# Performance work log

Measured on AMD Instinct MI355X. Metric: run time of the kernel, lower is better.

Reference implementation:

```python
import jax, jax.numpy as jnp
import numpy as np
import math

B, QL, HID = 4, 4, 4096          # batch, speculative q_len, hidden_size
NH, NKV, HD = 32, 8, 128         # attention heads, kv heads, head_dim
GROUPS = NH // NKV               # GQA repeat factor = 4
PRIOR = 4096                     # cached (prior) KV length
THETA = 1.0e6                    # Mixtral rope_theta


def setup_inputs() -> dict:
    key = jax.random.key(0)
    ks = jax.random.split(key, 7)
    hidden_states = jax.random.normal(ks[0], (B, QL, HID), jnp.float32)
    past_k = jax.random.normal(ks[1], (B, NKV, PRIOR, HD), jnp.float32)
    past_v = jax.random.normal(ks[2], (B, NKV, PRIOR, HD), jnp.float32)
    wq = jax.random.normal(ks[3], (HID, NH * HD), jnp.float32) * 0.02
    wk = jax.random.normal(ks[4], (HID, NKV * HD), jnp.float32) * 0.02
    wv = jax.random.normal(ks[5], (HID, NKV * HD), jnp.float32) * 0.02
    wo = jax.random.normal(ks[6], (NH * HD, HID), jnp.float32) * 0.02
    # prior mask: all cached positions visible
    attention_mask = jnp.ones((B, 1, QL, PRIOR), dtype=bool)
    # active mask: causal over the speculative window
    active_mask = jnp.broadcast_to(jnp.tril(jnp.ones((QL, QL), dtype=bool)), (B, 1, QL, QL))
    position_ids = jnp.broadcast_to(PRIOR + jnp.arange(QL, dtype=jnp.int64), (B, QL))
    return {"hidden_states": hidden_states, "past_k": past_k, "past_v": past_v,
            "wq": wq, "wk": wk, "wv": wv, "wo": wo,
            "attention_mask": attention_mask, "active_mask": active_mask,
            "position_ids": position_ids}


def _rotate_half(x):
    x1, x2 = jnp.split(x, 2, axis=-1)
    return jnp.concatenate([-x2, x1], axis=-1)


def _rope_cos_sin(position_ids):
    inv_freq = 1.0 / (THETA ** (jnp.arange(0, HD, 2, dtype=jnp.float32) / HD))  # [HD/2]
    freqs = position_ids.astype(jnp.float32)[..., None] * inv_freq              # [B,QL,HD/2]
    emb = jnp.concatenate([freqs, freqs], axis=-1)                              # [B,QL,HD]
    return jnp.cos(emb)[:, None], jnp.sin(emb)[:, None]                          # [B,1,QL,HD]


def reference(hidden_states, past_k, past_v, wq, wk, wv, wo,
              attention_mask, active_mask, position_ids):
    # fused QKV projection (no bias in Mixtral)
    q = (hidden_states @ wq).reshape(B, QL, NH, HD).transpose(0, 2, 1, 3)   # [B,NH,QL,HD]
    k = (hidden_states @ wk).reshape(B, QL, NKV, HD).transpose(0, 2, 1, 3)  # [B,NKV,QL,HD]
    v = (hidden_states @ wv).reshape(B, QL, NKV, HD).transpose(0, 2, 1, 3)
    # RoPE on Q and active K
    cos, sin = _rope_cos_sin(position_ids)
    q = q * cos + _rotate_half(q) * sin
    k = k * cos + _rotate_half(k) * sin
    # GQA repeat_kv
    k_prior = jnp.repeat(past_k, GROUPS, axis=1)  # [B,NH,PRIOR,HD]
    v_prior = jnp.repeat(past_v, GROUPS, axis=1)
    k_active = jnp.repeat(k, GROUPS, axis=1)      # [B,NH,QL,HD]
    v_active = jnp.repeat(v, GROUPS, axis=1)
    scale = 1.0 / math.sqrt(HD)
    neg = jnp.finfo(jnp.float32).min
    prior_scores = jnp.einsum('bhqd,bhkd->bhqk', q, k_prior) * scale
    prior_scores = jnp.where(attention_mask, prior_scores, neg)
    active_scores = jnp.einsum('bhqd,bhkd->bhqk', q, k_active) * scale
    active_scores = jnp.where(active_mask, active_scores, neg)   # is_speculation=True
    # decomposed softmax: shared max and shared divisor across prior/active
    max_score = jnp.maximum(prior_scores.max(-1, keepdims=True),
                            active_scores.max(-1, keepdims=True))
    prior_exp = jnp.exp(prior_scores - max_score)
    active_exp = jnp.exp(active_scores - max_score)
    divisor = prior_exp.sum(-1, keepdims=True) + active_exp.sum(-1, keepdims=True)
    attn = (jnp.einsum('bhqk,bhkd->bhqd', prior_exp / divisor, v_prior) +
            jnp.einsum('bhqk,bhkd->bhqd', active_exp / divisor, v_active))
    attn = attn.transpose(0, 2, 1, 3).reshape(B, QL, NH * HD)
    return attn @ wo
```

## Files before the change

kernel.cpp:

```cpp
#include <hip/hip_runtime.h>
#include <math.h>

#define NROWS 16
#define NCOLS 6144
#define HID   4096
#define NKV   8
#define HD    128
#define PRIOR 4096
#define NCH   32
#define CHUNK 128
#define SUB   64
#define KC1   128
#define NKC   32

__global__ __launch_bounds__(128)
void k_qkv_partial(const float* __restrict__ hid,
                   const float* __restrict__ wq,
                   const float* __restrict__ wk,
                   const float* __restrict__ wv,
                   float* __restrict__ part)
{
    const int t   = threadIdx.x;
    const int col = blockIdx.x * 256 + t * 2;
    const int kc  = blockIdx.y;
    const int k0  = kc * KC1;
    const float* w; int wn, wcol;
    if (col < 4096)      { w = wq; wn = 4096; wcol = col; }
    else if (col < 5120) { w = wk; wn = 1024; wcol = col - 4096; }
    else                 { w = wv; wn = 1024; wcol = col - 5120; }
    const float* wp = w + wcol + (size_t)k0 * wn;

    float acc[NROWS][2];
#pragma unroll
    for (int m = 0; m < NROWS; m++) { acc[m][0] = 0.f; acc[m][1] = 0.f; }
#pragma unroll 2
    for (int kk = 0; kk < KC1; kk += 4) {
        const float2 w0 = *(const float2*)(wp + (size_t)(kk + 0) * wn);
        const float2 w1 = *(const float2*)(wp + (size_t)(kk + 1) * wn);
        const float2 w2 = *(const float2*)(wp + (size_t)(kk + 2) * wn);
        const float2 w3 = *(const float2*)(wp + (size_t)(kk + 3) * wn);
#pragma unroll
        for (int m = 0; m < NROWS; m++) {
            const float4 h4 = *(const float4*)(hid + (size_t)m * HID + k0 + kk);
            acc[m][0] = fmaf(h4.x, w0.x, fmaf(h4.y, w1.x, fmaf(h4.z, w2.x, fmaf(h4.w, w3.x, acc[m][0]))));
            acc[m][1] = fmaf(h4.x, w0.y, fmaf(h4.y, w1.y, fmaf(h4.z, w2.y, fmaf(h4.w, w3.y, acc[m][1]))));
        }
    }
    float* po = part + (size_t)kc * (NROWS * NCOLS) + col;
#pragma unroll
    for (int m = 0; m < NROWS; m++)
        *(float2*)(po + (size_t)m * NCOLS) = make_float2(acc[m][0], acc[m][1]);
}

__global__ __launch_bounds__(256)
void k_reduce_rope(const float* __restrict__ part, float* __restrict__ qkv)
{
    const int tid = blockIdx.x * 256 + threadIdx.x;
    const double L64 = 0.21586735246819178;

    if (tid < 32768) {
        const int d = tid & 63, h = (tid >> 6) & 31, r = tid >> 11;
        const int c1 = h * HD + d;
        float s1 = 0.f, s2 = 0.f;
        for (int c = 0; c < NKC; c++) {
            const float* p = part + (size_t)c * (NROWS * NCOLS) + r * NCOLS + c1;
            s1 += p[0]; s2 += p[64];
        }
        const double ang = (double)(PRIOR + (r & 3)) * exp(-(double)d * L64);
        double sv, cv; sincos(ang, &sv, &cv);
        const float cf = (float)cv, sf = (float)sv, sc = 0.08838834764831845f;
        qkv[r * NCOLS + c1]      = (s1 * cf - s2 * sf) * sc;
        qkv[r * NCOLS + c1 + 64] = (s2 * cf + s1 * sf) * sc;
    } else if (tid < 40960) {
        const int idx = tid - 32768;
        const int d = idx & 63, kh = (idx >> 6) & 7, r = idx >> 9;
        const int c1 = 4096 + kh * HD + d;
        float s1 = 0.f, s2 = 0.f;
        for (int c = 0; c < NKC; c++) {
            const float* p = part + (size_t)c * (NROWS * NCOLS) + r * NCOLS + c1;
            s1 += p[0]; s2 += p[64];
        }
        const double ang = (double)(PRIOR + (r & 3)) * exp(-(double)d * L64);
        double sv, cv; sincos(ang, &sv, &cv);
        const float cf = (float)cv, sf = (float)sv;
        qkv[r * NCOLS + c1]      = s1 * cf - s2 * sf;
        qkv[r * NCOLS + c1 + 64] = s2 * cf + s1 * sf;
    } else {
        const int idx = tid - 40960;
        const int n = idx & 1023, r = idx >> 10;
        const int c1 = 5120 + n;
        float s = 0.f;
        for (int c = 0; c < NKC; c++)
            s += part[(size_t)c * (NROWS * NCOLS) + r * NCOLS + c1];
        qkv[r * NCOLS + c1] = s;
    }
}

__global__ __launch_bounds__(256, 4)
void k_attn_prior(const float* __restrict__ qkv,
                  const float* __restrict__ pk,
                  const float* __restrict__ pv,
                  float* __restrict__ part3)
{
    const int chunk = blockIdx.x, kvh = blockIdx.y, b = blockIdx.z;
    const int t = threadIdx.x;
    const int lane = t & 63;

    __shared__ float kT[128][64];
    __shared__ float qT[128][16];
    float* pP = &kT[88][0];
    float* aS = &kT[108][0];

    const int qt = t >> 6;
    const int h  = (lane >> 4) & 3;
    const int kt = lane & 15;

    const int d4pv = t & 31;
    const int kp   = (t >> 5) & 3;
    const int rh   = t >> 7;

    const size_t kvoff = ((size_t)(b * NKV + kvh) * PRIOR + (size_t)chunk * CHUNK) * HD;
    const float* kbase = pk + kvoff;
    const float* vbase = pv + kvoff;

    for (int i = t; i < 2048; i += 256) {
        const int r = i & 15, d = i >> 4;
        const int ql = r & 3, g = r >> 2;
        qT[d][r] = qkv[(size_t)(b * 4 + ql) * NCOLS + (kvh * 4 + g) * HD + d];
    }

    float m_r[4], l_r[4];
#pragma unroll
    for (int i = 0; i < 4; i++) { m_r[i] = -INFINITY; l_r[i] = 0.f; }
    float o[8][4];
#pragma unroll
    for (int jr = 0; jr < 8; jr++)
#pragma unroll
        for (int jd = 0; jd < 4; jd++) o[jr][jd] = 0.f;

    for (int st = 0; st < CHUNK / SUB; st++) {
        {
            const float* kr = kbase + (size_t)(st * SUB + lane) * HD + qt * 32;
#pragma unroll
            for (int i = 0; i < 8; i++) {
                const float4 k4 = *(const float4*)(kr + i * 4);
                const int d = qt * 32 + i * 4;
                kT[d + 0][lane] = k4.x; kT[d + 1][lane] = k4.y;
                kT[d + 2][lane] = k4.z; kT[d + 3][lane] = k4.w;
            }
        }
        __syncthreads();

        float a[4][4];
#pragma unroll
        for (int i = 0; i < 4; i++)
#pragma unroll
            for (int j = 0; j < 4; j++) a[i][j] = 0.f;
#pragma unroll 4
        for (int dd = 0; dd < 32; dd++) {
            const int d = h * 32 + dd;
            const float4 q4 = *(const float4*)(&qT[d][qt * 4]);
            const float4 k4 = *(const float4*)(&kT[d][kt * 4]);
            a[0][0]=fmaf(q4.x,k4.x,a[0][0]); a[0][1]=fmaf(q4.x,k4.y,a[0][1]); a[0][2]=fmaf(q4.x,k4.z,a[0][2]); a[0][3]=fmaf(q4.x,k4.w,a[0][3]);
            a[1][0]=fmaf(q4.y,k4.x,a[1][0]); a[1][1]=fmaf(q4.y,k4.y,a[1][1]); a[1][2]=fmaf(q4.y,k4.z,a[1][2]); a[1][3]=fmaf(q4.y,k4.w,a[1][3]);
            a[2][0]=fmaf(q4.z,k4.x,a[2][0]); a[2][1]=fmaf(q4.z,k4.y,a[2][1]); a[2][2]=fmaf(q4.z,k4.z,a[2][2]); a[2][3]=fmaf(q4.z,k4.w,a[2][3]);
            a[3][0]=fmaf(q4.w,k4.x,a[3][0]); a[3][1]=fmaf(q4.w,k4.y,a[3][1]); a[3][2]=fmaf(q4.w,k4.z,a[3][2]); a[3][3]=fmaf(q4.w,k4.w,a[3][3]);
        }
        __syncthreads();

#pragma unroll
        for (int i = 0; i < 4; i++)
#pragma unroll
            for (int j = 0; j < 4; j++) {
                float v = a[i][j];
                v += __shfl_xor(v, 16);
                v += __shfl_xor(v, 32);
                a[i][j] = v;
            }
        float al[4], pr[4][4];
#pragma unroll
        for (int i = 0; i < 4; i++) {
            float mx = fmaxf(fmaxf(a[i][0], a[i][1]), fmaxf(a[i][2], a[i][3]));
            mx = fmaxf(mx, __shfl_xor(mx, 1));
            mx = fmaxf(mx, __shfl_xor(mx, 2));
            mx = fmaxf(mx, __shfl_xor(mx, 4));
            mx = fmaxf(mx, __shfl_xor(mx, 8));
            const float mn = fmaxf(m_r[i], mx);
            al[i] = __expf(m_r[i] - mn);
            m_r[i] = mn;
            float s = 0.f;
#pragma unroll
            for (int j = 0; j < 4; j++) { pr[i][j] = __expf(a[i][j] - mn); s += pr[i][j]; }
            s += __shfl_xor(s, 1); s += __shfl_xor(s, 2);
            s += __shfl_xor(s, 4); s += __shfl_xor(s, 8);
            l_r[i] = l_r[i] * al[i] + s;
        }
        if (h == 0) {
#pragma unroll
            for (int j = 0; j < 4; j++)
                *(float4*)(pP + (kt * 4 + j) * 20 + qt * 4) =
                    make_float4(pr[0][j], pr[1][j], pr[2][j], pr[3][j]);
        }
        if (lane == 0) {
#pragma unroll
            for (int i = 0; i < 4; i++) aS[qt * 4 + i] = al[i];
        }
        __syncthreads();

        {
            float alv[8];
#pragma unroll
            for (int jr = 0; jr < 8; jr++) alv[jr] = aS[rh * 8 + jr];
#pragma unroll
            for (int jr = 0; jr < 8; jr++)
#pragma unroll
                for (int jd = 0; jd < 4; jd++) o[jr][jd] *= alv[jr];
            const float* vs = vbase + (size_t)st * SUB * HD + d4pv * 4;
#pragma unroll 4
            for (int j = 0; j < 16; j++) {
                const int key = kp * 16 + j;
                const float4 v4 = *(const float4*)(vs + (size_t)key * HD);
                const float4 pa = *(const float4*)(pP + key * 20 + rh * 8);
                const float4 pb = *(const float4*)(pP + key * 20 + rh * 8 + 4);
                const float pv8[8] = {pa.x, pa.y, pa.z, pa.w, pb.x, pb.y, pb.z, pb.w};
                const float vv[4] = {v4.x, v4.y, v4.z, v4.w};
#pragma unroll
                for (int jr = 0; jr < 8; jr++)
#pragma unroll
                    for (int jd = 0; jd < 4; jd++)
                        o[jr][jd] = fmaf(pv8[jr], vv[jd], o[jr][jd]);
            }
        }
        __syncthreads();
    }

    float* red = &kT[0][0];
    const int rb = (rh * 32 + d4pv) * 36;
    if (kp >= 2) {
        float* wdst = red + (kp - 2) * 2304 + rb;
#pragma unroll
        for (int jr = 0; jr < 8; jr++)
            *(float4*)(wdst + jr * 4) = make_float4(o[jr][0], o[jr][1], o[jr][2], o[jr][3]);
    }
    __syncthreads();
    if (kp < 2) {
        const float* rsrc = red + kp * 2304 + rb;
#pragma unroll
        for (int jr = 0; jr < 8; jr++) {
            const float4 x = *(const float4*)(rsrc + jr * 4);
            o[jr][0] += x.x; o[jr][1] += x.y; o[jr][2] += x.z; o[jr][3] += x.w;
        }
    }
    __syncthreads();
    if (kp == 1) {
        float* wdst = red + rb;
#pragma unroll
        for (int jr = 0; jr < 8; jr++)
            *(float4*)(wdst + jr * 4) = make_float4(o[jr][0], o[jr][1], o[jr][2], o[jr][3]);
    }
    __syncthreads();

    float* pout = part3 + (size_t)((b * NKV + kvh) * NCH + chunk) * 2080;
    if (lane == 0) {
#pragma unroll
        for (int i = 0; i < 4; i++) { pout[qt * 4 + i] = m_r[i]; pout[16 + qt * 4 + i] = l_r[i]; }
    }
    if (kp == 0) {
        const float* rsrc = red + rb;
#pragma unroll
        for (int jr = 0; jr < 8; jr++) {
            const float4 x = *(const float4*)(rsrc + jr * 4);
            *(float4*)(pout + 32 + (size_t)(rh * 8 + jr) * HD + d4pv * 4) =
                make_float4(o[jr][0] + x.x, o[jr][1] + x.y, o[jr][2] + x.z, o[jr][3] + x.w);
        }
    }
}

__global__ __launch_bounds__(256)
void k_combine(const float* __restrict__ qkv,
               const float* __restrict__ part3,
               float* __restrict__ attn)
{
    const int g = blockIdx.x & 3, kvh = (blockIdx.x >> 2) & 7, b = blockIdx.x >> 5;
    const int t = threadIdx.x;
    __shared__ float qL[4][128], kA[4][128], vA[4][128];
    __shared__ float mC[NCH][4], lC[NCH][4], fC[NCH][4];
    __shared__ float sAct[4][4], pA[4][4], invL[4];

    for (int i = t; i < 512; i += 256) {
        const int ql = i >> 7, d = i & 127;
        qL[ql][d] = qkv[(size_t)(b * 4 + ql) * NCOLS + (kvh * 4 + g) * HD + d];
        kA[ql][d] = qkv[(size_t)(b * 4 + ql) * NCOLS + 4096 + kvh * HD + d];
        vA[ql][d] = qkv[(size_t)(b * 4 + ql) * NCOLS + 5120 + kvh * HD + d];
    }
    const float* p3 = part3 + (size_t)(b * NKV + kvh) * NCH * 2080;
    for (int i = t; i < NCH * 4; i += 256) {
        const int c = i >> 2, lr = i & 3;
        mC[c][lr] = p3[c * 2080 + g * 4 + lr];
        lC[c][lr] = p3[c * 2080 + 16 + g * 4 + lr];
    }
    __syncthreads();
    if (t < 16) {
        const int lr = t >> 2, k = t & 3;
        float s = 0.f;
        for (int d = 0; d < HD; d++) s = fmaf(qL[lr][d], kA[k][d], s);
        sAct[lr][k] = s;
    }
    __syncthreads();
    if (t < 4) {
        const int lr = t;
        float M = -INFINITY;
        for (int c = 0; c < NCH; c++) M = fmaxf(M, mC[c][lr]);
        for (int k = 0; k <= lr; k++) M = fmaxf(M, sAct[lr][k]);
        float l = 0.f;
        for (int c = 0; c < NCH; c++) {
            const float f = __expf(mC[c][lr] - M);
            fC[c][lr] = f;
            l = fmaf(f, lC[c][lr], l);
        }
#pragma unroll
        for (int k = 0; k < 4; k++) {
            const float p = (k <= lr) ? __expf(sAct[lr][k] - M) : 0.f;
            pA[lr][k] = p; l += p;
        }
        invL[lr] = 1.f / l;
    }
    __syncthreads();

    const int d = t & 127, hr = t >> 7;
    const int lr0 = hr * 2, lr1 = hr * 2 + 1;
    float o0 = 0.f, o1 = 0.f;
    for (int c = 0; c < NCH; c++) {
        const float f0 = fC[c][lr0], f1 = fC[c][lr1];
        const float* pa = p3 + c * 2080 + 32 + (g * 4 + lr0) * HD + d;
        o0 = fmaf(f0, pa[0],  o0);
        o1 = fmaf(f1, pa[HD], o1);
    }
#pragma unroll
    for (int k = 0; k < 4; k++) {
        const float v = vA[k][d];
        o0 = fmaf(pA[lr0][k], v, o0);
        o1 = fmaf(pA[lr1][k], v, o1);
    }
    attn[(size_t)(b * 4 + lr0) * HID + (kvh * 4 + g) * HD + d] = o0 * invL[lr0];
    attn[(size_t)(b * 4 + lr1) * HID + (kvh * 4 + g) * HD + d] = o1 * invL[lr1];
}

__global__ __launch_bounds__(128)
void k_out_partial(const float* __restrict__ attn,
                   const float* __restrict__ wo,
                   float* __restrict__ part)
{
    const int t = threadIdx.x;
    const int col = blockIdx.x * 256 + t * 2;
    const int kc = blockIdx.y;
    const int k0 = kc * KC1;
    const float* wp = wo + col + (size_t)k0 * HID;

    float acc[NROWS][2];
#pragma unroll
    for (int m = 0; m < NROWS; m++) { acc[m][0] = 0.f; acc[m][1] = 0.f; }
#pragma unroll 2
    for (int kk = 0; kk < KC1; kk += 4) {
        const float2 w0 = *(const float2*)(wp + (size_t)(kk + 0) * HID);
        const float2 w1 = *(const float2*)(wp + (size_t)(kk + 1) * HID);
        const float2 w2 = *(const float2*)(wp + (size_t)(kk + 2) * HID);
        const float2 w3 = *(const float2*)(wp + (size_t)(kk + 3) * HID);
#pragma unroll
        for (int m = 0; m < NROWS; m++) {
            const float4 h4 = *(const float4*)(attn + (size_t)m * HID + k0 + kk);
            acc[m][0] = fmaf(h4.x, w0.x, fmaf(h4.y, w1.x, fmaf(h4.z, w2.x, fmaf(h4.w, w3.x, acc[m][0]))));
            acc[m][1] = fmaf(h4.x, w0.y, fmaf(h4.y, w1.y, fmaf(h4.z, w2.y, fmaf(h4.w, w3.y, acc[m][1]))));
        }
    }
    float* po = part + (size_t)kc * (NROWS * HID) + col;
#pragma unroll
    for (int m = 0; m < NROWS; m++)
        *(float2*)(po + (size_t)m * HID) = make_float2(acc[m][0], acc[m][1]);
}

__global__ __launch_bounds__(256)
void k_out_reduce(const float* __restrict__ part, float* __restrict__ out)
{
    const int tid = blockIdx.x * 256 + threadIdx.x;
    const float* p = part + (size_t)tid * 4;
    float4 s = make_float4(0.f, 0.f, 0.f, 0.f);
    for (int c = 0; c < NKC; c++) {
        const float4 a = *(const float4*)(p + (size_t)c * (NROWS * HID));
        s.x += a.x; s.y += a.y; s.z += a.z; s.w += a.w;
    }
    *(float4*)(out + (size_t)tid * 4) = s;
}

extern "C" void kernel_launch(void* const* d_in, const int* in_sizes, int n_in,
                              void* d_out, int out_size, void* d_ws, size_t ws_size,
                              hipStream_t stream)
{
    (void)in_sizes; (void)n_in; (void)out_size; (void)ws_size;
    const float* hid = (const float*)d_in[0];
    const float* pk  = (const float*)d_in[1];
    const float* pv  = (const float*)d_in[2];
    const float* wq  = (const float*)d_in[3];
    const float* wk  = (const float*)d_in[4];
    const float* wv  = (const float*)d_in[5];
    const float* wo  = (const float*)d_in[6];
    float* out = (float*)d_out;
    float* ws  = (float*)d_ws;

    float* P1   = ws;
    float* P3   = ws;
    float* P5   = ws;
    float* qkv  = ws + 3145728;
    float* attn = ws + 3244032;

    k_qkv_partial<<<dim3(24, NKC), 128, 0, stream>>>(hid, wq, wk, wv, P1);
    k_reduce_rope<<<224, 256, 0, stream>>>(P1, qkv);
    k_attn_prior<<<dim3(NCH, NKV, 4), 256, 0, stream>>>(qkv, pk, pv, P3);
    k_combine<<<128, 256, 0, stream>>>(qkv, P3, attn);
    k_out_partial<<<dim3(16, NKC), 128, 0, stream>>>(attn, wo, P5);
    k_out_reduce<<<64, 256, 0, stream>>>(P5, out);
}
```

Before: 321.3 us.

## Restructure prior attention PV to wave-local readlane broadcast, prefetch K, parallelize merge

The prior-attention kernel no longer stages probabilities in shared memory and reduces partial outputs across thread groups. Each wave now keeps its own 4 query rows and broadcasts probabilities with readlane, so V is read directly and most barriers plus the final shared-memory reduction go away. K for the next subtile is prefetched into registers, and the merge kernel's active-score and softmax-merge steps now run across 128 threads using shuffles instead of 16 or 4 threads. Several loop unroll factors also increase, at the cost of more register pressure and redundant V loads per wave.

```diff
diff --git a/kernel.cpp b/kernel.cpp
--- a/kernel.cpp
+++ b/kernel.cpp
@@ -13,6 +13,10 @@
 #define KC1   128
 #define NKC   32
 
+__device__ __forceinline__ float rdlane(float v, int l) {
+    return __int_as_float(__builtin_amdgcn_readlane(__float_as_int(v), l));
+}
+
 __global__ __launch_bounds__(128)
 void k_qkv_partial(const float* __restrict__ hid,
                    const float* __restrict__ wq,
@@ -33,7 +37,7 @@
     float acc[NROWS][2];
 #pragma unroll
     for (int m = 0; m < NROWS; m++) { acc[m][0] = 0.f; acc[m][1] = 0.f; }
-#pragma unroll 2
+#pragma unroll 4
     for (int kk = 0; kk < KC1; kk += 4) {
         const float2 w0 = *(const float2*)(wp + (size_t)(kk + 0) * wn);
         const float2 w1 = *(const float2*)(wp + (size_t)(kk + 1) * wn);
@@ -62,6 +66,7 @@
         const int d = tid & 63, h = (tid >> 6) & 31, r = tid >> 11;
         const int c1 = h * HD + d;
         float s1 = 0.f, s2 = 0.f;
+#pragma unroll 8
         for (int c = 0; c < NKC; c++) {
             const float* p = part + (size_t)c * (NROWS * NCOLS) + r * NCOLS + c1;
             s1 += p[0]; s2 += p[64];
@@ -76,6 +81,7 @@
         const int d = idx & 63, kh = (idx >> 6) & 7, r = idx >> 9;
         const int c1 = 4096 + kh * HD + d;
         float s1 = 0.f, s2 = 0.f;
+#pragma unroll 8
         for (int c = 0; c < NKC; c++) {
             const float* p = part + (size_t)c * (NROWS * NCOLS) + r * NCOLS + c1;
             s1 += p[0]; s2 += p[64];
@@ -90,6 +96,7 @@
         const int n = idx & 1023, r = idx >> 10;
         const int c1 = 5120 + n;
         float s = 0.f;
+#pragma unroll 8
         for (int c = 0; c < NKC; c++)
             s += part[(size_t)c * (NROWS * NCOLS) + r * NCOLS + c1];
         qkv[r * NCOLS + c1] = s;
@@ -108,20 +115,21 @@
 
     __shared__ float kT[128][64];
     __shared__ float qT[128][16];
-    float* pP = &kT[88][0];
-    float* aS = &kT[108][0];
 
     const int qt = t >> 6;
     const int h  = (lane >> 4) & 3;
     const int kt = lane & 15;
 
-    const int d4pv = t & 31;
-    const int kp   = (t >> 5) & 3;
-    const int rh   = t >> 7;
-
     const size_t kvoff = ((size_t)(b * NKV + kvh) * PRIOR + (size_t)chunk * CHUNK) * HD;
     const float* kbase = pk + kvoff;
     const float* vbase = pv + kvoff;
+
+    float4 kreg[8];
+    {
+        const float* kr = kbase + (size_t)lane * HD + qt * 32;
+#pragma unroll
+        for (int i = 0; i < 8; i++) kreg[i] = *(const float4*)(kr + i * 4);
+    }
 
     for (int i = t; i < 2048; i += 256) {
         const int r = i & 15, d = i >> 4;
@@ -129,25 +137,21 @@
         qT[d][r] = qkv[(size_t)(b * 4 + ql) * NCOLS + (kvh * 4 + g) * HD + d];
     }
 
-    float m_r[4], l_r[4];
-#pragma unroll
-    for (int i = 0; i < 4; i++) { m_r[i] = -INFINITY; l_r[i] = 0.f; }
-    float o[8][4];
-#pragma unroll
-    for (int jr = 0; jr < 8; jr++)
-#pragma unroll
-        for (int jd = 0; jd < 4; jd++) o[jr][jd] = 0.f;
+    float m_r[4], l_r[4], o[4][2];
+#pragma unroll
+    for (int i = 0; i < 4; i++) { m_r[i] = -INFINITY; l_r[i] = 0.f; o[i][0] = 0.f; o[i][1] = 0.f; }
 
     for (int st = 0; st < CHUNK / SUB; st++) {
-        {
-            const float* kr = kbase + (size_t)(st * SUB + lane) * HD + qt * 32;
-#pragma unroll
-            for (int i = 0; i < 8; i++) {
-                const float4 k4 = *(const float4*)(kr + i * 4);
-                const int d = qt * 32 + i * 4;
-                kT[d + 0][lane] = k4.x; kT[d + 1][lane] = k4.y;
-                kT[d + 2][lane] = k4.z; kT[d + 3][lane] = k4.w;
-            }
+#pragma unroll
+        for (int i = 0; i < 8; i++) {
+            const int d = qt * 32 + i * 4;
+            kT[d + 0][lane] = kreg[i].x; kT[d + 1][lane] = kreg[i].y;
+            kT[d + 2][lane] = kreg[i].z; kT[d + 3][lane] = kreg[i].w;
+        }
+        if (st == 0) {
+            const float* kr = kbase + (size_t)(SUB + lane) * HD + qt * 32;
+#pragma unroll
+            for (int i = 0; i < 8; i++) kreg[i] = *(const float4*)(kr + i * 4);
         }
         __syncthreads();
 
@@ -195,85 +199,39 @@
             s += __shfl_xor(s, 4); s += __shfl_xor(s, 8);
             l_r[i] = l_r[i] * al[i] + s;
         }
-        if (h == 0) {
-#pragma unroll
-            for (int j = 0; j < 4; j++)
-                *(float4*)(pP + (kt * 4 + j) * 20 + qt * 4) =
-                    make_float4(pr[0][j], pr[1][j], pr[2][j], pr[3][j]);
-        }
-        if (lane == 0) {
-#pragma unroll
-            for (int i = 0; i < 4; i++) aS[qt * 4 + i] = al[i];
-        }
-        __syncthreads();
-
-        {
-            float alv[8];
-#pragma unroll
-            for (int jr = 0; jr < 8; jr++) alv[jr] = aS[rh * 8 + jr];
-#pragma unroll
-            for (int jr = 0; jr < 8; jr++)
-#pragma unroll
-                for (int jd = 0; jd < 4; jd++) o[jr][jd] *= alv[jr];
-            const float* vs = vbase + (size_t)st * SUB * HD + d4pv * 4;
-#pragma unroll 4
-            for (int j = 0; j < 16; j++) {
-                const int key = kp * 16 + j;
-                const float4 v4 = *(const float4*)(vs + (size_t)key * HD);
-                const float4 pa = *(const float4*)(pP + key * 20 + rh * 8);
-                const float4 pb = *(const float4*)(pP + key * 20 + rh * 8 + 4);
-                const float pv8[8] = {pa.x, pa.y, pa.z, pa.w, pb.x, pb.y, pb.z, pb.w};
-                const float vv[4] = {v4.x, v4.y, v4.z, v4.w};
-#pragma unroll
-                for (int jr = 0; jr < 8; jr++)
-#pragma unroll
-                    for (int jd = 0; jd < 4; jd++)
-                        o[jr][jd] = fmaf(pv8[jr], vv[jd], o[jr][jd]);
+#pragma unroll
+        for (int i = 0; i < 4; i++) { o[i][0] *= al[i]; o[i][1] *= al[i]; }
+
+        const float* vs = vbase + (size_t)st * SUB * HD + (lane << 1);
+#pragma unroll
+        for (int g4 = 0; g4 < 16; g4++) {
+            const float2 v0 = *(const float2*)(vs + (size_t)(g4 * 4 + 0) * HD);
+            const float2 v1 = *(const float2*)(vs + (size_t)(g4 * 4 + 1) * HD);
+            const float2 v2 = *(const float2*)(vs + (size_t)(g4 * 4 + 2) * HD);
+            const float2 v3 = *(const float2*)(vs + (size_t)(g4 * 4 + 3) * HD);
+#pragma unroll
+            for (int i = 0; i < 4; i++) {
+                const float p0 = rdlane(pr[i][0], g4);
+                const float p1 = rdlane(pr[i][1], g4);
+                const float p2 = rdlane(pr[i][2], g4);
+                const float p3v = rdlane(pr[i][3], g4);
+                o[i][0] = fmaf(p0,  v0.x, o[i][0]); o[i][1] = fmaf(p0,  v0.y, o[i][1]);
+                o[i][0] = fmaf(p1,  v1.x, o[i][0]); o[i][1] = fmaf(p1,  v1.y, o[i][1]);
+                o[i][0] = fmaf(p2,  v2.x, o[i][0]); o[i][1] = fmaf(p2,  v2.y, o[i][1]);
+                o[i][0] = fmaf(p3v, v3.x, o[i][0]); o[i][1] = fmaf(p3v, v3.y, o[i][1]);
             }
         }
-        __syncthreads();
-    }
-
-    float* red = &kT[0][0];
-    const int rb = (rh * 32 + d4pv) * 36;
-    if (kp >= 2) {
-        float* wdst = red + (kp - 2) * 2304 + rb;
-#pragma unroll
-        for (int jr = 0; jr < 8; jr++)
-            *(float4*)(wdst + jr * 4) = make_float4(o[jr][0], o[jr][1], o[jr][2], o[jr][3]);
-    }
-    __syncthreads();
-    if (kp < 2) {
-        const float* rsrc = red + kp * 2304 + rb;
-#pragma unroll
-        for (int jr = 0; jr < 8; jr++) {
-            const float4 x = *(const float4*)(rsrc + jr * 4);
-            o[jr][0] += x.x; o[jr][1] += x.y; o[jr][2] += x.z; o[jr][3] += x.w;
-        }
-    }
-    __syncthreads();
-    if (kp == 1) {
-        float* wdst = red + rb;
-#pragma unroll
-        for (int jr = 0; jr < 8; jr++)
-            *(float4*)(wdst + jr * 4) = make_float4(o[jr][0], o[jr][1], o[jr][2], o[jr][3]);
-    }
-    __syncthreads();
+    }
 
     float* pout = part3 + (size_t)((b * NKV + kvh) * NCH + chunk) * 2080;
     if (lane == 0) {
 #pragma unroll
         for (int i = 0; i < 4; i++) { pout[qt * 4 + i] = m_r[i]; pout[16 + qt * 4 + i] = l_r[i]; }
     }
-    if (kp == 0) {
-        const float* rsrc = red + rb;
-#pragma unroll
-        for (int jr = 0; jr < 8; jr++) {
-            const float4 x = *(const float4*)(rsrc + jr * 4);
-            *(float4*)(pout + 32 + (size_t)(rh * 8 + jr) * HD + d4pv * 4) =
-                make_float4(o[jr][0] + x.x, o[jr][1] + x.y, o[jr][2] + x.z, o[jr][3] + x.w);
-        }
-    }
+#pragma unroll
+    for (int i = 0; i < 4; i++)
+        *(float2*)(pout + 32 + (size_t)(qt * 4 + i) * HD + (lane << 1)) =
+            make_float2(o[i][0], o[i][1]);
 }
 
 __global__ __launch_bounds__(256)
@@ -300,36 +258,43 @@
         lC[c][lr] = p3[c * 2080 + 16 + g * 4 + lr];
     }
     __syncthreads();
-    if (t < 16) {
-        const int lr = t >> 2, k = t & 3;
+    if (t < 128) {
+        const int pp = t >> 3, dd = t & 7;
+        const int lr = pp >> 2, k = pp & 3;
         float s = 0.f;
-        for (int d = 0; d < HD; d++) s = fmaf(qL[lr][d], kA[k][d], s);
-        sAct[lr][k] = s;
+#pragma unroll
+        for (int d = 0; d < 16; d++)
+            s = fmaf(qL[lr][dd * 16 + d], kA[k][dd * 16 + d], s);
+        s += __shfl_xor(s, 1); s += __shfl_xor(s, 2); s += __shfl_xor(s, 4);
+        if (dd == 0) sAct[lr][k] = s;
     }
     __syncthreads();
-    if (t < 4) {
-        const int lr = t;
-        float M = -INFINITY;
-        for (int c = 0; c < NCH; c++) M = fmaxf(M, mC[c][lr]);
-        for (int k = 0; k <= lr; k++) M = fmaxf(M, sAct[lr][k]);
-        float l = 0.f;
-        for (int c = 0; c < NCH; c++) {
-            const float f = __expf(mC[c][lr] - M);
-            fC[c][lr] = f;
-            l = fmaf(f, lC[c][lr], l);
-        }
-#pragma unroll
-        for (int k = 0; k < 4; k++) {
-            const float p = (k <= lr) ? __expf(sAct[lr][k] - M) : 0.f;
-            pA[lr][k] = p; l += p;
-        }
-        invL[lr] = 1.f / l;
+    if (t < 128) {
+        const int lr = t >> 5, c = t & 31;
+        const float m  = mC[c][lr];
+        const bool act = (c < 4) && (c <= lr);
+        const float sa = act ? sAct[lr][c] : -INFINITY;
+        float M = fmaxf(m, sa);
+        M = fmaxf(M, __shfl_xor(M, 1));
+        M = fmaxf(M, __shfl_xor(M, 2));
+        M = fmaxf(M, __shfl_xor(M, 4));
+        M = fmaxf(M, __shfl_xor(M, 8));
+        M = fmaxf(M, __shfl_xor(M, 16));
+        const float f = __expf(m - M);
+        fC[c][lr] = f;
+        const float pact = act ? __expf(sa - M) : 0.f;
+        if (c < 4) pA[lr][c] = pact;
+        float l = fmaf(f, lC[c][lr], pact);
+        l += __shfl_xor(l, 1); l += __shfl_xor(l, 2);
+        l += __shfl_xor(l, 4); l += __shfl_xor(l, 8); l += __shfl_xor(l, 16);
+        if (c == 0) invL[lr] = 1.f / l;
     }
     __syncthreads();
 
     const int d = t & 127, hr = t >> 7;
     const int lr0 = hr * 2, lr1 = hr * 2 + 1;
     float o0 = 0.f, o1 = 0.f;
+#pragma unroll 4
     for (int c = 0; c < NCH; c++) {
         const float f0 = fC[c][lr0], f1 = fC[c][lr1];
         const float* pa = p3 + c * 2080 + 32 + (g * 4 + lr0) * HD + d;
@@ -360,7 +325,7 @@
     float acc[NROWS][2];
 #pragma unroll
     for (int m = 0; m < NROWS; m++) { acc[m][0] = 0.f; acc[m][1] = 0.f; }
-#pragma unroll 2
+#pragma unroll 4
     for (int kk = 0; kk < KC1; kk += 4) {
         const float2 w0 = *(const float2*)(wp + (size_t)(kk + 0) * HID);
         const float2 w1 = *(const float2*)(wp + (size_t)(kk + 1) * HID);
@@ -385,6 +350,7 @@
     const int tid = blockIdx.x * 256 + threadIdx.x;
     const float* p = part + (size_t)tid * 4;
     float4 s = make_float4(0.f, 0.f, 0.f, 0.f);
+#pragma unroll 8
     for (int c = 0; c < NKC; c++) {
         const float4 a = *(const float4*)(p + (size_t)c * (NROWS * HID));
         s.x += a.x; s.y += a.y; s.z += a.z; s.w += a.w;
```

Result: slower. 328.7 us (+2.3%).
